# Performance work log

Measured on AMD Instinct MI355X. Metric: run time of the kernel, lower is better.

Reference implementation:

```python
import jax, jax.numpy as jnp
import numpy as np


def _depthwise3x3(x_nhwc, w):
    # w: (3, 3, 1, C) — depthwise conv, padding=1, matches torch Conv2d(groups=C)
    return jax.lax.conv_general_dilated(
        x_nhwc, w, window_strides=(1, 1), padding='SAME',
        dimension_numbers=('NHWC', 'HWIO', 'NHWC'),
        feature_group_count=x_nhwc.shape[-1])


def _stripe_attn(q, k, v, lepe_w, B, H, W, nh, hd, ss, axis, scale):
    # q/k/v: (B, H, W, nh*hd); axis 0 = horizontal stripes, 1 = vertical
    pad_h = (-H) % ss if axis == 0 else 0
    pad_w = (-W) % ss if axis == 1 else 0
    if pad_h or pad_w:
        pad = ((0, 0), (0, pad_h), (0, pad_w), (0, 0))
        q, k, v = jnp.pad(q, pad), jnp.pad(k, pad), jnp.pad(v, pad)
    Hp, Wp = q.shape[1], q.shape[2]
    lepe = _depthwise3x3(v, lepe_w)  # (B, Hp, Wp, nh*hd)

    if axis == 0:
        nS = Hp // ss
        def to_win(t):  # -> (B*nS*Wp, nh, ss, hd)
            t = t.reshape(B, nS, ss, Wp, nh, hd)
            return t.transpose(0, 1, 3, 4, 2, 5).reshape(B * nS * Wp, nh, ss, hd)
    else:
        nS = Wp // ss
        def to_win(t):  # -> (B*Hp*nS, nh, ss, hd)
            t = t.reshape(B, Hp, nS, ss, nh, hd)
            return t.transpose(0, 1, 2, 4, 3, 5).reshape(B * Hp * nS, nh, ss, hd)

    qw, kw, vw, lw = to_win(q), to_win(k), to_win(v), to_win(lepe)
    attn = jax.nn.softmax(jnp.einsum('wnqd,wnkd->wnqk', qw, kw) / scale, axis=-1)
    out = jnp.einsum('wnqk,wnkd->wnqd', attn, vw) + lw  # (Wnum, nh, ss, hd)

    if axis == 0:
        out = out.transpose(0, 2, 1, 3).reshape(B, nS, Wp, ss, nh * hd)
        out = out.transpose(0, 1, 3, 2, 4).reshape(B, Hp, Wp, nh * hd)
    else:
        out = out.transpose(0, 2, 1, 3).reshape(B, Hp, nS, ss, nh * hd)
        out = out.reshape(B, Hp, Wp, nh * hd)
    return out[:, :H, :W, :].reshape(B, H * W, nh * hd)


def setup_inputs() -> dict:
    key = jax.random.key(0)
    ks = jax.random.split(key, 6)
    B, H, W, dim, n_heads, ss = 8, 64, 64, 512, 16, 8
    half = dim // 2
    x = jax.random.normal(ks[0], (B, H * W, dim), dtype=jnp.float32)
    w_qkv = jax.random.normal(ks[1], (3 * dim, dim), dtype=jnp.float32) * 0.02
    w_proj = jax.random.normal(ks[2], (dim, dim), dtype=jnp.float32) * 0.02
    b_proj = jnp.zeros((dim,), dtype=jnp.float32)
    lepe_h_w = jax.random.normal(ks[3], (3, 3, 1, half), dtype=jnp.float32) * 0.1
    lepe_v_w = jax.random.normal(ks[4], (3, 3, 1, half), dtype=jnp.float32) * 0.1
    return {"x": x, "w_qkv": w_qkv, "w_proj": w_proj, "b_proj": b_proj,
            "lepe_h_w": lepe_h_w, "lepe_v_w": lepe_v_w, "H": H, "W": W}


def reference(x, w_qkv, w_proj, b_proj, lepe_h_w, lepe_v_w, H, W):
    B, L, C = x.shape
    n_heads, ss = 16, 8
    hd = C // n_heads
    scale = float(np.sqrt(hd))
    qkv = x @ w_qkv.T  # (B, L, 3C)
    q, k, v = jnp.split(qkv, 3, axis=-1)
    q = q.reshape(B, H, W, C)
    k = k.reshape(B, H, W, C)
    v = v.reshape(B, H, W, C)
    half = C // 2
    nh_h = n_heads // 2
    nh_v = n_heads - nh_h
    out_h = _stripe_attn(q[..., :half], k[..., :half], v[..., :half],
                         lepe_h_w, B, H, W, nh_h, hd, ss, axis=0, scale=scale)
    out_v = _stripe_attn(q[..., half:], k[..., half:], v[..., half:],
                         lepe_v_w, B, H, W, nh_v, hd, ss, axis=1, scale=scale)
    out = jnp.concatenate([out_h, out_v], axis=-1)
    return out @ w_proj.T + b_proj
```

## Files before the change

### kernel.cpp

```cpp
#include <hip/hip_runtime.h>
#include <hip/hip_bf16.h>
#include <stdint.h>

typedef _Float16 half2v __attribute__((ext_vector_type(2)));
typedef _Float16 half8v __attribute__((ext_vector_type(8)));
typedef uint32_t u32x4  __attribute__((ext_vector_type(4)));
typedef float    f32x4  __attribute__((ext_vector_type(4)));

__device__ __forceinline__ unsigned short f2h(float f) {
  _Float16 h = (_Float16)f;
  return __builtin_bit_cast(unsigned short, h);
}
__device__ __forceinline__ half2v bch2(uint32_t u) {
  return __builtin_bit_cast(half2v, u);
}
__device__ __forceinline__ uint32_t pkrtz_u32(float a, float b) {
  return __builtin_bit_cast(uint32_t, __builtin_amdgcn_cvt_pkrtz(a, b));
}

__device__ __forceinline__ int qkv_idx(int half, int b, int n, int h, int w) {
  int idx = half * 8388608 + (b * 8 + n) * 131072;
  idx += (half == 0) ? ((h >> 3) * 16384 + w * 256 + (h & 7) * 32)
                     : (h * 2048 + w * 32);
  return idx;
}

#define GLOAD_LDS16(gsrc, lbase)                                          \
  __builtin_amdgcn_global_load_lds(                                       \
      (const __attribute__((address_space(1))) uint32_t*)(gsrc),          \
      (__attribute__((address_space(3))) uint32_t*)(lbase), 16, 0, 0)

__global__ __launch_bounds__(256) void cvt_all(
    const float* __restrict__ x,
    const float* __restrict__ wqkv, const float* __restrict__ wproj,
    const float* __restrict__ lh,   const float* __restrict__ lv,
    unsigned short* __restrict__ ox,
    unsigned short* __restrict__ owqkv, unsigned short* __restrict__ owproj,
    unsigned short* __restrict__ owlep)
{
  int i = blockIdx.x * 256 + threadIdx.x;
  const float* src; unsigned short* dst; int off;
  if (i < 4194304)      { src = x;     dst = ox;           off = i; }
  else if ((i -= 4194304) < 196608) { src = wqkv;  dst = owqkv;  off = i; }
  else if ((i -= 196608) < 65536)   { src = wproj; dst = owproj; off = i; }
  else if ((i -= 65536) < 576)      { src = lh;    dst = owlep;  off = i; }
  else if ((i -= 576) < 576)        { src = lv;    dst = owlep + 2304; off = i; }
  else return;
  float4 f = reinterpret_cast<const float4*>(src)[off];
  ushort4 u;
  u.x = f2h(f.x); u.y = f2h(f.y); u.z = f2h(f.z); u.w = f2h(f.w);
  reinterpret_cast<ushort4*>(dst)[off] = u;
}

__global__ __launch_bounds__(512, 2) void gemm8p(
    const unsigned short* __restrict__ A,
    const unsigned short* __restrict__ Bm,
    unsigned short* __restrict__ Cq)
{
  constexpr int K = 512;
  constexpr int NIT = 4;
  __shared__ unsigned short As[2][256 * 64];
  __shared__ unsigned short Bs[2][256 * 64];
  const int tid  = threadIdx.x;
  const int cpx  = gridDim.x >> 3;
  const int bid  = blockIdx.x;
  const int wgid = (bid & 7) * cpx + (bid >> 3);
  const int mt   = wgid >> 1;
  const int nh   = wgid & 1;
  const int m0   = mt * 256;
  const int wave = tid >> 6, lane = tid & 63;
  const int wr  = wave >> 2;
  const int wcn = wave & 3;

  const int srow = tid >> 3;
  const int schk = ((tid & 7) ^ (srow & 7)) * 8;
  const size_t aSrc = (size_t)(m0 + srow) * K + schk;
  size_t bSrc = (size_t)(nh * 768 + srow) * K + schk;
  char* ldsA = (char*)(&As[0][0]) + (tid & ~63) * 16;
  char* ldsB = (char*)(&Bs[0][0]) + (tid & ~63) * 16;

#define SA_U(b, kt, u)                                                      \
  GLOAD_LDS16(A + aSrc + (size_t)(u) * 64 * K + (size_t)(kt) * 64,          \
              ldsA + (b) * 32768 + (u) * 8192)
#define SB_U(b, kt, u, bS)                                                  \
  GLOAD_LDS16(Bm + (bS) + (size_t)(u) * 64 * K + (size_t)(kt) * 64,         \
              ldsB + (b) * 32768 + (u) * 8192)
#define BARS                                                                \
  __builtin_amdgcn_s_barrier();                                             \
  __builtin_amdgcn_sched_barrier(0)

  SA_U(0, 0, 0); SA_U(0, 0, 1); SA_U(0, 0, 2); SA_U(0, 0, 3);
  SB_U(0, 0, 0, bSrc); SB_U(0, 0, 1, bSrc); SB_U(0, 0, 2, bSrc); SB_U(0, 0, 3, bSrc);
  SB_U(1, 1, 0, bSrc); SB_U(1, 1, 1, bSrc); SB_U(1, 1, 2, bSrc); SB_U(1, 1, 3, bSrc);
  asm volatile("s_waitcnt vmcnt(4)" ::: "memory");
  BARS;

  const int lr  = lane & 15;
  const int kg  = lane >> 4;
  const int ck0 = kg ^ (lr & 7);

#define LD_AF(buf, mg, ks)                                                  \
  do {                                                                      \
    const unsigned short* ap = &As[buf][0] +                                \
        (wr * 128 + (mg) * 64 + lr) * 64 + (((ks) ? (ck0 ^ 4) : ck0)) * 8;  \
    af[0] = *(const half8v*)(ap);                                           \
    af[1] = *(const half8v*)(ap + 1024);                                    \
    af[2] = *(const half8v*)(ap + 2048);                                    \
    af[3] = *(const half8v*)(ap + 3072);                                    \
  } while (0)
#define LD_BF(buf, ks)                                                      \
  do {                                                                      \
    const unsigned short* bp = &Bs[buf][0] +                                \
        (wcn * 64 + lr) * 64 + (((ks) ? (ck0 ^ 4) : ck0)) * 8;              \
    bf[0] = *(const half8v*)(bp);                                           \
    bf[1] = *(const half8v*)(bp + 1024);                                    \
    bf[2] = *(const half8v*)(bp + 2048);                                    \
    bf[3] = *(const half8v*)(bp + 3072);                                    \
  } while (0)
#define MROW(mg, i)                                                         \
  acc[(mg)*4+(i)][0] = __builtin_amdgcn_mfma_f32_16x16x32_f16(bf[0], af[i], acc[(mg)*4+(i)][0], 0, 0, 0); \
  acc[(mg)*4+(i)][1] = __builtin_amdgcn_mfma_f32_16x16x32_f16(bf[1], af[i], acc[(mg)*4+(i)][1], 0, 0, 0); \
  acc[(mg)*4+(i)][2] = __builtin_amdgcn_mfma_f32_16x16x32_f16(bf[2], af[i], acc[(mg)*4+(i)][2], 0, 0, 0); \
  acc[(mg)*4+(i)][3] = __builtin_amdgcn_mfma_f32_16x16x32_f16(bf[3], af[i], acc[(mg)*4+(i)][3], 0, 0, 0);
#define MFMA16(mg)                                                          \
  do {                                                                      \
    __builtin_amdgcn_s_setprio(1);                                          \
    MROW(mg, 0); MROW(mg, 1); MROW(mg, 2); MROW(mg, 3);                     \
    __builtin_amdgcn_s_setprio(0);                                          \
  } while (0)

  f32x4 acc[8][4];
  const f32x4 zero = {0.f, 0.f, 0.f, 0.f};

  #pragma unroll 1
  for (int pass = 0; pass < 3; ++pass) {
    const int n0 = (nh * 3 + pass) * 256;
    #pragma unroll
    for (int i = 0; i < 8; ++i)
      #pragma unroll
      for (int j = 0; j < 4; ++j) acc[i][j] = zero;

    for (int it2 = 0; it2 < NIT; ++it2) {
      const bool more = (it2 + 1 < NIT);
      const int keven = 2 * it2;
      half8v af[4], bf[4];
      LD_BF(0, 0); LD_AF(0, 0, 0);
      SA_U(1, keven + 1, 0); SA_U(1, keven + 1, 1);
      BARS;
      MFMA16(0);
      BARS;
      LD_AF(0, 1, 0);
      SA_U(1, keven + 1, 2); SA_U(1, keven + 1, 3);
      BARS;
      MFMA16(1);
      BARS;
      LD_BF(0, 1); LD_AF(0, 0, 1);
      BARS;
      MFMA16(0);
      BARS;
      LD_AF(0, 1, 1);
      if (more) {
        SB_U(0, keven + 2, 0, bSrc); SB_U(0, keven + 2, 1, bSrc);
        asm volatile("s_waitcnt vmcnt(2)" ::: "memory");
      } else {
        asm volatile("s_waitcnt vmcnt(0)" ::: "memory");
      }
      BARS;
      MFMA16(1);
      BARS;
      LD_BF(1, 0); LD_AF(1, 0, 0);
      if (more) { SB_U(0, keven + 2, 2, bSrc); SB_U(0, keven + 2, 3, bSrc); }
      BARS;
      MFMA16(0);
      BARS;
      LD_AF(1, 1, 0);
      if (more) { SA_U(0, keven + 2, 0); SA_U(0, keven + 2, 1); }
      BARS;
      MFMA16(1);
      BARS;
      LD_BF(1, 1); LD_AF(1, 0, 1);
      if (more) { SA_U(0, keven + 2, 2); SA_U(0, keven + 2, 3); }
      BARS;
      MFMA16(0);
      BARS;
      LD_AF(1, 1, 1);
      if (more) {
        SB_U(1, keven + 3, 0, bSrc); SB_U(1, keven + 3, 1, bSrc);
        SB_U(1, keven + 3, 2, bSrc); SB_U(1, keven + 3, 3, bSrc);
        asm volatile("s_waitcnt vmcnt(4)" ::: "memory");
      }
      BARS;
      MFMA16(1);
      BARS;
    }

    if (pass < 2) {
      const size_t bSrcN = bSrc + (size_t)256 * K;
      SA_U(0, 0, 0); SA_U(0, 0, 1); SA_U(0, 0, 2); SA_U(0, 0, 3);
      SB_U(0, 0, 0, bSrcN); SB_U(0, 0, 1, bSrcN); SB_U(0, 0, 2, bSrcN); SB_U(0, 0, 3, bSrcN);
      SB_U(1, 1, 0, bSrcN); SB_U(1, 1, 1, bSrcN); SB_U(1, 1, 2, bSrcN); SB_U(1, 1, 3, bSrcN);
      bSrc = bSrcN;
    }

    {
      const int cr = (lane >> 4) * 4;
      const int cc = lane & 15;
      const int mb   = m0 + wr * 128;
      const int btok = mb >> 12;
      const int hr0  = (mb >> 6) & 63;
      #pragma unroll
      for (int j = 0; j < 4; ++j) {
        const int nb    = n0 + wcn * 64 + j * 16 + cr;
        const int tq    = nb >> 9;
        const int halfc = (nb >> 8) & 1;
        const int nn    = (nb & 255) >> 5;
        const int ch4   = nb & 31;
        const int headbase = tq * 16777216 + halfc * 8388608 +
                             (btok * 8 + nn) * 131072 + ch4;
        #pragma unroll
        for (int i = 0; i < 8; ++i) {
          const int hrow = hr0 + (i >> 2);
          const int wpix = (i & 3) * 16 + cc;
          const int off = halfc ? (hrow * 2048 + wpix * 32)
                                : ((hrow >> 3) * 16384 + wpix * 256 + (hrow & 7) * 32);
          uint2 r;
          r.x = pkrtz_u32(acc[i][j][0], acc[i][j][1]);
          r.y = pkrtz_u32(acc[i][j][2], acc[i][j][3]);
          *reinterpret_cast<uint2*>(Cq + headbase + off) = r;
        }
      }
    }

    if (pass < 2) {
      asm volatile("s_waitcnt vmcnt(0)" ::: "memory");
      BARS;
    }
  }
#undef SA_U
#undef SB_U
#undef LD_AF
#undef LD_BF
#undef MROW
#undef MFMA16
#undef BARS
}

__global__ __launch_bounds__(256) void gemm_proj(
    const unsigned short* __restrict__ A,
    const unsigned short* __restrict__ B,
    float* __restrict__ Cf,
    const float* __restrict__ bias)
{
  constexpr int K = 512, N = 512;
  __shared__ unsigned short As[2][128 * 32];
  __shared__ unsigned short Bs[2][128 * 32];
  const int tid  = threadIdx.x;
  const int gn   = N >> 7;
  const int cpx  = gridDim.x >> 3;
  const int bid  = blockIdx.x;
  const int wgid = (bid & 7) * cpx + (bid >> 3);
  const int m0   = (wgid / gn) * 128;
  const int n0   = (wgid % gn) * 128;
  const int wave = tid >> 6, lane = tid & 63;
  const int wr = wave >> 1, wc = wave & 1;
  const int sr = tid >> 2;
  const int sc = ((tid & 3) ^ ((tid >> 3) & 3)) * 8;
  const size_t aBase0 = (size_t)(m0 + sr) * K + sc;
  const size_t aBase1 = (size_t)(m0 + 64 + sr) * K + sc;
  const size_t bBase0 = (size_t)(n0 + sr) * K + sc;
  const size_t bBase1 = (size_t)(n0 + 64 + sr) * K + sc;
  char* ldsA = (char*)(&As[0][0]) + (tid & ~63) * 16;
  char* ldsB = (char*)(&Bs[0][0]) + (tid & ~63) * 16;

#define STAGE_P(bsel, kofs)                                        \
  do {                                                             \
    GLOAD_LDS16(A + aBase0 + (kofs), ldsA + (bsel) * 8192);        \
    GLOAD_LDS16(A + aBase1 + (kofs), ldsA + (bsel) * 8192 + 4096); \
    GLOAD_LDS16(B + bBase0 + (kofs), ldsB + (bsel) * 8192);        \
    GLOAD_LDS16(B + bBase1 + (kofs), ldsB + (bsel) * 8192 + 4096); \
  } while (0)

  STAGE_P(0, 0);

  f32x4 acc[4][4];
  const f32x4 zero = {0.f, 0.f, 0.f, 0.f};
  #pragma unroll
  for (int i = 0; i < 4; ++i)
    #pragma unroll
    for (int j = 0; j < 4; ++j) acc[i][j] = zero;

  const int lr   = lane & 15;
  const int slot = (lane >> 4) ^ ((lr >> 1) & 3);

  auto compute = [&](const unsigned short* Asb, const unsigned short* Bsb) {
    half8v af[4], bfr[4];
    #pragma unroll
    for (int i = 0; i < 4; ++i)
      af[i] = *reinterpret_cast<const half8v*>(Asb + (wr * 64 + i * 16 + lr) * 32 + slot * 8);
    #pragma unroll
    for (int j = 0; j < 4; ++j)
      bfr[j] = *reinterpret_cast<const half8v*>(Bsb + (wc * 64 + j * 16 + lr) * 32 + slot * 8);
    __builtin_amdgcn_s_setprio(1);
    #pragma unroll
    for (int i = 0; i < 4; ++i)
      #pragma unroll
      for (int j = 0; j < 4; ++j)
        acc[i][j] = __builtin_amdgcn_mfma_f32_16x16x32_f16(bfr[j], af[i], acc[i][j], 0, 0, 0);
    __builtin_amdgcn_s_setprio(0);
  };

  const int nt = K >> 5;
  for (int t = 0; t < nt - 1; ++t) {
    STAGE_P((t + 1) & 1, (t + 1) * 32);
    asm volatile("s_waitcnt vmcnt(4)" ::: "memory");
    __builtin_amdgcn_s_barrier();
    __builtin_amdgcn_sched_barrier(0);
    compute(&As[t & 1][0], &Bs[t & 1][0]);
    __builtin_amdgcn_s_barrier();
    __builtin_amdgcn_sched_barrier(0);
  }
  asm volatile("s_waitcnt vmcnt(0)" ::: "memory");
  __builtin_amdgcn_s_barrier();
  __builtin_amdgcn_sched_barrier(0);
  compute(&As[(nt - 1) & 1][0], &Bs[(nt - 1) & 1][0]);
#undef STAGE_P

  const int cr = (lane >> 4) * 4;
  const int cc = lane & 15;
  #pragma unroll
  for (int j = 0; j < 4; ++j) {
    const int n = n0 + wc * 64 + j * 16 + cr;
    const float4 b4 = *reinterpret_cast<const float4*>(bias + n);
    #pragma unroll
    for (int i = 0; i < 4; ++i) {
      const int m = m0 + wr * 64 + i * 16 + cc;
      float4 r;
      r.x = acc[i][j][0] + b4.x;
      r.y = acc[i][j][1] + b4.y;
      r.z = acc[i][j][2] + b4.z;
      r.w = acc[i][j][3] + b4.w;
      *reinterpret_cast<float4*>(Cf + (size_t)m * N + n) = r;
    }
  }
}

__global__ __launch_bounds__(256) void attn_lepe(
    const unsigned short* __restrict__ qkvp,
    const unsigned short* __restrict__ wlep,
    unsigned short* __restrict__ outp)
{
  const int gw   = (int)((blockIdx.x * 256 + threadIdx.x) >> 6);
  const int lane = threadIdx.x & 63;
  const int half = gw >> 14;
  const int id   = gw & 16383;
  const int b    = id >> 11;
  const int n    = (id >> 8) & 7;
  int h0, w0;
  if (half == 0) { h0 = ((id >> 5) & 7) * 8; w0 = (id & 31) * 2; }
  else           { h0 = ((id >> 3) & 31) * 2; w0 = (id & 7) * 8; }
  const int baseA = qkv_idx(half, b, n, h0, w0);
  const int dWin  = (half == 0) ? 256 : 2048;
  const int baseB = baseA + dWin;

  const int qr = lane >> 3, kr = lane & 7;
  const unsigned short* qA = qkvp + baseA + qr * 32;
  const unsigned short* kA = qkvp + 16777216 + baseA + kr * 32;
  float sA = 0.f, sB = 0.f;
  #pragma unroll
  for (int c = 0; c < 4; ++c) {
    const u32x4 qa = *reinterpret_cast<const u32x4*>(qA + c * 8);
    const u32x4 ka = *reinterpret_cast<const u32x4*>(kA + c * 8);
    const u32x4 qb = *reinterpret_cast<const u32x4*>(qA + dWin + c * 8);
    const u32x4 kb = *reinterpret_cast<const u32x4*>(kA + dWin + c * 8);
    #pragma unroll
    for (int e = 0; e < 4; ++e) {
      sA = __builtin_amdgcn_fdot2(bch2(qa[e]), bch2(ka[e]), sA, false);
      sB = __builtin_amdgcn_fdot2(bch2(qb[e]), bch2(kb[e]), sB, false);
    }
  }
  const float scl = 0.17677669529663687f;
  const float pA = __expf(sA * scl);
  const float pB = __expf(sB * scl);
  float denA = pA, denB = pB;
  denA += __shfl_xor(denA, 1); denA += __shfl_xor(denA, 2); denA += __shfl_xor(denA, 4);
  denB += __shfl_xor(denB, 1); denB += __shfl_xor(denB, 2); denB += __shfl_xor(denB, 4);
  const float aAv = pA * __builtin_amdgcn_rcpf(denA);
  const float aBv = pB * __builtin_amdgcn_rcpf(denB);
  const uint32_t adu = pkrtz_u32(aAv, aBv);

  const int dgrp = lane & 3;
  const int win  = (lane >> 2) & 1;
  const int qr2  = lane >> 3;
  const int d0   = dgrp * 8;
  const int mybase = win ? baseB : baseA;
  const unsigned short* vwin = qkvp + 33554432 + mybase;

  half2v o01 = {0,0}, o23 = {0,0}, o45 = {0,0}, o67 = {0,0};
  #pragma unroll
  for (int k = 0; k < 8; ++k) {
    const uint32_t pairw = (uint32_t)__shfl((int)adu, qr2 * 8 + k);
    const half2v ph = bch2(pairw);
    const _Float16 av = win ? ph.y : ph.x;
    const half2v ak2 = {av, av};
    const u32x4 vv = *reinterpret_cast<const u32x4*>(vwin + k * 32 + d0);
    o01 += ak2 * bch2(vv[0]);
    o23 += ak2 * bch2(vv[1]);
    o45 += ak2 * bch2(vv[2]);
    o67 += ak2 * bch2(vv[3]);
  }

  const int hq = (half == 0) ? (h0 + qr2) : (h0 + win);
  const int wq = (half == 0) ? (w0 + win) : (w0 + qr2);
  const unsigned short* vplane = qkvp + 33554432;
  const unsigned short* wl = wlep + half * 2304 + n * 32 + d0;
  half2v l01 = {0,0}, l23 = {0,0}, l45 = {0,0}, l67 = {0,0};
  #pragma unroll
  for (int dy = -1; dy <= 1; ++dy) {
    #pragma unroll
    for (int dx = -1; dx <= 1; ++dx) {
      const int hh = hq + dy, ww = wq + dx;
      u32x4 vv = {0u, 0u, 0u, 0u};
      if ((unsigned)hh < 64u && (unsigned)ww < 64u)
        vv = *reinterpret_cast<const u32x4*>(vplane + qkv_idx(half, b, n, hh, ww) + d0);
      const u32x4 wt = *reinterpret_cast<const u32x4*>(wl + ((dy + 1) * 3 + dx + 1) * 256);
      l01 += bch2(wt[0]) * bch2(vv[0]);
      l23 += bch2(wt[1]) * bch2(vv[1]);
      l45 += bch2(wt[2]) * bch2(vv[2]);
      l67 += bch2(wt[3]) * bch2(vv[3]);
    }
  }

  const int m = b * 4096 + hq * 64 + wq;
  const int chan0 = half * 256 + n * 32;
  u32x4 r;
  r[0] = __builtin_bit_cast(uint32_t, (half2v)(o01 + l01));
  r[1] = __builtin_bit_cast(uint32_t, (half2v)(o23 + l23));
  r[2] = __builtin_bit_cast(uint32_t, (half2v)(o45 + l45));
  r[3] = __builtin_bit_cast(uint32_t, (half2v)(o67 + l67));
  *reinterpret_cast<u32x4*>(outp + (size_t)m * 512 + chan0 + d0) = r;
}

extern "C" void kernel_launch(void* const* d_in, const int* in_sizes, int n_in,
                              void* d_out, int out_size, void* d_ws, size_t ws_size,
                              hipStream_t stream) {
  const float* x      = (const float*)d_in[0];
  const float* w_qkv  = (const float*)d_in[1];
  const float* w_proj = (const float*)d_in[2];
  const float* b_proj = (const float*)d_in[3];
  const float* lepe_h = (const float*)d_in[4];
  const float* lepe_v = (const float*)d_in[5];
  float* out = (float*)d_out;

  char* ws = (char*)d_ws;
  unsigned short* qkv_p   = (unsigned short*)ws;
  unsigned short* xh      = (unsigned short*)(ws + 100663296);
  unsigned short* wqkv_h  = (unsigned short*)(ws + 134217728);
  unsigned short* wproj_h = (unsigned short*)(ws + 135790592);
  unsigned short* wlep_h  = (unsigned short*)(ws + 136314880);

  cvt_all<<<17413, 256, 0, stream>>>(x, w_qkv, w_proj, lepe_h, lepe_v,
                                     xh, wqkv_h, wproj_h, wlep_h);

  gemm8p<<<256, 512, 0, stream>>>(xh, wqkv_h, qkv_p);

  attn_lepe<<<8192, 256, 0, stream>>>(qkv_p, wlep_h, xh);

  gemm_proj<<<1024, 256, 0, stream>>>(xh, wproj_h, out, b_proj);
}
```

Measured before the change: 169.8 us.

## Fuse x fp32-to-fp16 conversion into QKV GEMM A-tile loading

Drops the separate conversion pass over the activation tensor x. The QKV GEMM now reads fp32 x directly into registers, converts it with packed round-to-zero conversions, and writes fp16 into LDS, replacing the direct global-to-LDS loads for A. This removes a full write and reread of a 32MB fp16 copy plus part of a kernel launch. In exchange, the GEMM reads twice the A bytes, uses more registers to stage them, and adds extra LDS-write waits inside the pipelined loop. Each x tile is re-read by all three N passes, so the fp32 traffic is paid several times.

```diff
diff --git a/kernel.cpp b/kernel.cpp
--- a/kernel.cpp
+++ b/kernel.cpp
@@ -30,21 +30,18 @@
       (const __attribute__((address_space(1))) uint32_t*)(gsrc),          \
       (__attribute__((address_space(3))) uint32_t*)(lbase), 16, 0, 0)
 
-__global__ __launch_bounds__(256) void cvt_all(
-    const float* __restrict__ x,
+__global__ __launch_bounds__(256) void cvt_weights(
     const float* __restrict__ wqkv, const float* __restrict__ wproj,
     const float* __restrict__ lh,   const float* __restrict__ lv,
-    unsigned short* __restrict__ ox,
     unsigned short* __restrict__ owqkv, unsigned short* __restrict__ owproj,
     unsigned short* __restrict__ owlep)
 {
   int i = blockIdx.x * 256 + threadIdx.x;
   const float* src; unsigned short* dst; int off;
-  if (i < 4194304)      { src = x;     dst = ox;           off = i; }
-  else if ((i -= 4194304) < 196608) { src = wqkv;  dst = owqkv;  off = i; }
-  else if ((i -= 196608) < 65536)   { src = wproj; dst = owproj; off = i; }
-  else if ((i -= 65536) < 576)      { src = lh;    dst = owlep;  off = i; }
-  else if ((i -= 576) < 576)        { src = lv;    dst = owlep + 2304; off = i; }
+  if      (i < 196608) { src = wqkv;  dst = owqkv;        off = i; }
+  else if (i < 262144) { src = wproj; dst = owproj;       off = i - 196608; }
+  else if (i < 262720) { src = lh;    dst = owlep;        off = i - 262144; }
+  else if (i < 263296) { src = lv;    dst = owlep + 2304; off = i - 262720; }
   else return;
   float4 f = reinterpret_cast<const float4*>(src)[off];
   ushort4 u;
@@ -53,7 +50,7 @@
 }
 
 __global__ __launch_bounds__(512, 2) void gemm8p(
-    const unsigned short* __restrict__ A,
+    const float* __restrict__ X,
     const unsigned short* __restrict__ Bm,
     unsigned short* __restrict__ Cq)
 {
@@ -76,12 +73,31 @@
   const int schk = ((tid & 7) ^ (srow & 7)) * 8;
   const size_t aSrc = (size_t)(m0 + srow) * K + schk;
   size_t bSrc = (size_t)(nh * 768 + srow) * K + schk;
-  char* ldsA = (char*)(&As[0][0]) + (tid & ~63) * 16;
   char* ldsB = (char*)(&Bs[0][0]) + (tid & ~63) * 16;
-
-#define SA_U(b, kt, u)                                                      \
-  GLOAD_LDS16(A + aSrc + (size_t)(u) * 64 * K + (size_t)(kt) * 64,          \
-              ldsA + (b) * 32768 + (u) * 8192)
+  unsigned short* const aw = &As[0][0] + tid * 8;
+
+  float4 ar[4][2];
+
+#define ALOAD(kt)                                                           \
+  do {                                                                      \
+    _Pragma("unroll")                                                       \
+    for (int u = 0; u < 4; ++u) {                                           \
+      ar[u][0] = *reinterpret_cast<const float4*>(X + aSrc + (size_t)u * 64 * K + (size_t)(kt) * 64);     \
+      ar[u][1] = *reinterpret_cast<const float4*>(X + aSrc + (size_t)u * 64 * K + (size_t)(kt) * 64 + 4); \
+    }                                                                       \
+  } while (0)
+#define AWRITE(b)                                                           \
+  do {                                                                      \
+    _Pragma("unroll")                                                       \
+    for (int u = 0; u < 4; ++u) {                                           \
+      u32x4 w;                                                              \
+      w[0] = pkrtz_u32(ar[u][0].x, ar[u][0].y);                             \
+      w[1] = pkrtz_u32(ar[u][0].z, ar[u][0].w);                             \
+      w[2] = pkrtz_u32(ar[u][1].x, ar[u][1].y);                             \
+      w[3] = pkrtz_u32(ar[u][1].z, ar[u][1].w);                             \
+      *reinterpret_cast<u32x4*>(aw + (b) * 16384 + u * 4096) = w;           \
+    }                                                                       \
+  } while (0)
 #define SB_U(b, kt, u, bS)                                                  \
   GLOAD_LDS16(Bm + (bS) + (size_t)(u) * 64 * K + (size_t)(kt) * 64,         \
               ldsB + (b) * 32768 + (u) * 8192)
@@ -89,10 +105,12 @@
   __builtin_amdgcn_s_barrier();                                             \
   __builtin_amdgcn_sched_barrier(0)
 
-  SA_U(0, 0, 0); SA_U(0, 0, 1); SA_U(0, 0, 2); SA_U(0, 0, 3);
+  ALOAD(0);
   SB_U(0, 0, 0, bSrc); SB_U(0, 0, 1, bSrc); SB_U(0, 0, 2, bSrc); SB_U(0, 0, 3, bSrc);
   SB_U(1, 1, 0, bSrc); SB_U(1, 1, 1, bSrc); SB_U(1, 1, 2, bSrc); SB_U(1, 1, 3, bSrc);
-  asm volatile("s_waitcnt vmcnt(4)" ::: "memory");
+  asm volatile("s_waitcnt vmcnt(8)" ::: "memory");
+  AWRITE(0);
+  asm volatile("s_waitcnt vmcnt(4) lgkmcnt(0)" ::: "memory");
   BARS;
 
   const int lr  = lane & 15;
@@ -145,12 +163,11 @@
       const int keven = 2 * it2;
       half8v af[4], bf[4];
       LD_BF(0, 0); LD_AF(0, 0, 0);
-      SA_U(1, keven + 1, 0); SA_U(1, keven + 1, 1);
+      ALOAD(keven + 1);
       BARS;
       MFMA16(0);
       BARS;
       LD_AF(0, 1, 0);
-      SA_U(1, keven + 1, 2); SA_U(1, keven + 1, 3);
       BARS;
       MFMA16(1);
       BARS;
@@ -165,6 +182,8 @@
       } else {
         asm volatile("s_waitcnt vmcnt(0)" ::: "memory");
       }
+      AWRITE(1);
+      asm volatile("s_waitcnt lgkmcnt(0)" ::: "memory");
       BARS;
       MFMA16(1);
       BARS;
@@ -174,12 +193,11 @@
       MFMA16(0);
       BARS;
       LD_AF(1, 1, 0);
-      if (more) { SA_U(0, keven + 2, 0); SA_U(0, keven + 2, 1); }
+      if (more) ALOAD(keven + 2);
       BARS;
       MFMA16(1);
       BARS;
       LD_BF(1, 1); LD_AF(1, 0, 1);
-      if (more) { SA_U(0, keven + 2, 2); SA_U(0, keven + 2, 3); }
       BARS;
       MFMA16(0);
       BARS;
@@ -188,6 +206,8 @@
         SB_U(1, keven + 3, 0, bSrc); SB_U(1, keven + 3, 1, bSrc);
         SB_U(1, keven + 3, 2, bSrc); SB_U(1, keven + 3, 3, bSrc);
         asm volatile("s_waitcnt vmcnt(4)" ::: "memory");
+        AWRITE(0);
+        asm volatile("s_waitcnt lgkmcnt(0)" ::: "memory");
       }
       BARS;
       MFMA16(1);
@@ -196,7 +216,7 @@
 
     if (pass < 2) {
       const size_t bSrcN = bSrc + (size_t)256 * K;
-      SA_U(0, 0, 0); SA_U(0, 0, 1); SA_U(0, 0, 2); SA_U(0, 0, 3);
+      ALOAD(0);
       SB_U(0, 0, 0, bSrcN); SB_U(0, 0, 1, bSrcN); SB_U(0, 0, 2, bSrcN); SB_U(0, 0, 3, bSrcN);
       SB_U(1, 1, 0, bSrcN); SB_U(1, 1, 1, bSrcN); SB_U(1, 1, 2, bSrcN); SB_U(1, 1, 3, bSrcN);
       bSrc = bSrcN;
@@ -233,10 +253,13 @@
 
     if (pass < 2) {
       asm volatile("s_waitcnt vmcnt(0)" ::: "memory");
-      BARS;
-    }
-  }
-#undef SA_U
+      AWRITE(0);
+      asm volatile("s_waitcnt lgkmcnt(0)" ::: "memory");
+      BARS;
+    }
+  }
+#undef ALOAD
+#undef AWRITE
 #undef SB_U
 #undef LD_AF
 #undef LD_BF
@@ -453,17 +476,17 @@
 
   char* ws = (char*)d_ws;
   unsigned short* qkv_p   = (unsigned short*)ws;
-  unsigned short* xh      = (unsigned short*)(ws + 100663296);
+  unsigned short* ah      = (unsigned short*)(ws + 100663296);
   unsigned short* wqkv_h  = (unsigned short*)(ws + 134217728);
   unsigned short* wproj_h = (unsigned short*)(ws + 135790592);
   unsigned short* wlep_h  = (unsigned short*)(ws + 136314880);
 
-  cvt_all<<<17413, 256, 0, stream>>>(x, w_qkv, w_proj, lepe_h, lepe_v,
-                                     xh, wqkv_h, wproj_h, wlep_h);
-
-  gemm8p<<<256, 512, 0, stream>>>(xh, wqkv_h, qkv_p);
-
-  attn_lepe<<<8192, 256, 0, stream>>>(qkv_p, wlep_h, xh);
-
-  gemm_proj<<<1024, 256, 0, stream>>>(xh, wproj_h, out, b_proj);
-}
+  cvt_weights<<<1029, 256, 0, stream>>>(w_qkv, w_proj, lepe_h, lepe_v,
+                                        wqkv_h, wproj_h, wlep_h);
+
+  gemm8p<<<256, 512, 0, stream>>>(x, wqkv_h, qkv_p);
+
+  attn_lepe<<<8192, 256, 0, stream>>>(qkv_p, wlep_h, ah);
+
+  gemm_proj<<<1024, 256, 0, stream>>>(ah, wproj_h, out, b_proj);
+}
```

Result: slower. 181.6 us (+7.0%).
